# Performance work log

Hardware: AMD Instinct MI355X
Metric: run time of the kernel (lower is better)

The kernel has to match this reference:

```python
import jax, jax.numpy as jnp
import numpy as np

B, S, D, H = 4, 2048, 1024, 16
DK = D // H

def setup_inputs() -> dict:
    key = jax.random.key(0)
    ks = jax.random.split(key, 12)
    s = 1.0 / np.sqrt(D)
    return {
        "query": jax.random.normal(ks[0], (B, S, D), jnp.float32),
        "key": jax.random.normal(ks[1], (B, S, D), jnp.float32),
        "value": jax.random.normal(ks[2], (B, S, D), jnp.float32),
        "mask": jax.random.randint(ks[3], (B, S, S), 0, 2, jnp.int32),
        "Wq": jax.random.normal(ks[4], (D, D), jnp.float32) * s,
        "bq": jnp.zeros((D,), jnp.float32),
        "Wk": jax.random.normal(ks[5], (D, D), jnp.float32) * s,
        "bk": jnp.zeros((D,), jnp.float32),
        "Wv": jax.random.normal(ks[6], (D, D), jnp.float32) * s,
        "bv": jnp.zeros((D,), jnp.float32),
        "Wo": jax.random.normal(ks[7], (D, D), jnp.float32) * s,
        "bo": jnp.zeros((D,), jnp.float32),
    }

def _split_heads(x):
    b, s, _ = x.shape
    return x.reshape(b, s, H, DK).transpose(0, 2, 1, 3)  # [b,h,s,dk]

def reference(query, key, value, mask, Wq, bq, Wk, bk, Wv, bv, Wo, bo):
    # torch nn.Linear: y = x @ W.T + b
    Q = _split_heads(query @ Wq.T + bq)
    K = _split_heads(key @ Wk.T + bk)
    V = _split_heads(value @ Wv.T + bv)
    scores = jnp.einsum('bhqd,bhkd->bhqk', Q, K) / np.sqrt(DK)
    scores = jnp.where(mask[:, None, :, :] == 0, jnp.float32(-1e9), scores)
    probs = jax.nn.softmax(scores, axis=-1)
    attn = jnp.einsum('bhqk,bhkd->bhqd', probs, V)
    out = attn.transpose(0, 2, 1, 3).reshape(query.shape[0], -1, H * DK)
    return out @ Wo.T + bo
```

## Files before the change

kernel.cpp:

```cpp
#include <hip/hip_runtime.h>

typedef __attribute__((ext_vector_type(8))) short short8;
typedef __attribute__((ext_vector_type(8))) unsigned short ushort8_t;
typedef __attribute__((ext_vector_type(4))) float floatx4;
typedef __attribute__((ext_vector_type(2))) _Float16 half2_t;
typedef __attribute__((ext_vector_type(4))) _Float16 half4;
typedef __attribute__((ext_vector_type(8))) _Float16 half8;

#define B_ 4
#define S_ 2048
#define D_ 1024
#define H_ 16
#define DK_ 64
#define BS_ (B_ * S_)

union V8u { half8 v8; half4 v4[2]; };
union H16 { _Float16 h; unsigned short u; };

typedef const __attribute__((address_space(1))) void* gvp;
typedef __attribute__((address_space(3))) void* lvp;

static __device__ __forceinline__ unsigned short f2bf(float f) {
  union { float f; unsigned int u; } x; x.f = f;
  unsigned int r = x.u + 0x7fffu + ((x.u >> 16) & 1u);
  return (unsigned short)(r >> 16);
}

static __device__ __forceinline__ half2_t pk_f16(float a, float b) {
  return __builtin_bit_cast(half2_t, __builtin_amdgcn_cvt_pkrtz(a, b));
}

__global__ void cast3_kernel(const float* __restrict__ a, const float* __restrict__ b,
                             const float* __restrict__ c,
                             unsigned short* __restrict__ oa, unsigned short* __restrict__ ob,
                             unsigned short* __restrict__ oc, int n4) {
  int i = blockIdx.x * blockDim.x + threadIdx.x;
  int w = blockIdx.y;
  const float* src = (w == 0) ? a : (w == 1) ? b : c;
  unsigned short* dst = (w == 0) ? oa : (w == 1) ? ob : oc;
  if (i < n4) {
    float4 v = ((const float4*)src)[i];
    ushort4 o;
    o.x = f2bf(v.x); o.y = f2bf(v.y); o.z = f2bf(v.z); o.w = f2bf(v.w);
    ((ushort4*)dst)[i] = o;
  }
}

__global__ void cast4_kernel(const float* __restrict__ a, const float* __restrict__ b,
                             const float* __restrict__ c, const float* __restrict__ d,
                             unsigned short* __restrict__ oa, unsigned short* __restrict__ ob,
                             unsigned short* __restrict__ oc, unsigned short* __restrict__ od, int n4) {
  int i = blockIdx.x * blockDim.x + threadIdx.x;
  int w = blockIdx.y;
  const float* src = (w == 0) ? a : (w == 1) ? b : (w == 2) ? c : d;
  unsigned short* dst = (w == 0) ? oa : (w == 1) ? ob : (w == 2) ? oc : od;
  if (i < n4) {
    float4 v = ((const float4*)src)[i];
    ushort4 o;
    o.x = f2bf(v.x); o.y = f2bf(v.y); o.z = f2bf(v.z); o.w = f2bf(v.w);
    ((ushort4*)dst)[i] = o;
  }
}

__global__ void pack_mask(const int* __restrict__ mask, unsigned long long* __restrict__ bits) {
  int i = blockIdx.x * blockDim.x + threadIdx.x;
  unsigned long long m = __ballot(mask[i] != 0);
  if ((threadIdx.x & 63) == 0) bits[i >> 6] = m;
}

__global__ void transpose_v(const unsigned short* __restrict__ Vh, unsigned short* __restrict__ Vt) {
  __shared__ unsigned short T[64][72];
  int bh = blockIdx.y;
  int s0 = blockIdx.x * 64;
  int tid = threadIdx.x;
  int r = tid >> 3, c = (tid & 7) * 8;
  const unsigned short* src = Vh + ((size_t)bh * S_ + s0) * DK_;
#pragma unroll
  for (int p = 0; p < 2; ++p)
    *(uint4*)(&T[r + p * 32][c]) = *(const uint4*)(src + (size_t)(r + p * 32) * DK_ + c);
  __syncthreads();
  unsigned short* dst = Vt + (size_t)bh * DK_ * S_;
#pragma unroll
  for (int p = 0; p < 2; ++p) {
    int d = r + p * 32;
    ushort8_t o;
#pragma unroll
    for (int i = 0; i < 8; ++i) {
      int pos = c + i;
      int th = pos >> 5, rem = pos & 31;
      int q4 = rem >> 3, rem2 = rem & 7;
      int t = th * 2 + (rem2 >> 2), j = rem2 & 3;
      int k = t * 16 + q4 * 4 + j;
      o[i] = T[k][d];
    }
    *(ushort8_t*)(dst + (size_t)d * S_ + s0 + c) = o;
  }
}

__device__ __forceinline__ void gemm_core(
    const unsigned short* __restrict__ X, const unsigned short* __restrict__ W,
    const float* __restrict__ bias, void* __restrict__ Y,
    float scale, int mode, int bm, int bn,
    unsigned short* As, unsigned short* Bs)
{
  constexpr int K = D_, N = D_;
  int tid = threadIdx.x;
  int wave = tid >> 6, lane = tid & 63, quad = lane >> 4, li = lane & 15;
  int wm = wave >> 1, wn = wave & 1;
  int srow = lane >> 3;
  int scol = ((lane & 7) ^ srow) * 8;
  const unsigned short* gA = X + (size_t)(bm * 128 + wave * 32 + srow) * K + scol;
  const unsigned short* gB = W + (size_t)(bn * 128 + wave * 32 + srow) * K + scol;

  auto stage = [&](int buf, int k0) {
#pragma unroll
    for (int j = 0; j < 4; ++j) {
      __builtin_amdgcn_global_load_lds((gvp)(gA + (size_t)(j * 8) * K + k0),
          (lvp)(As + buf * 8192 + wave * 2048 + j * 512), 16, 0, 0);
      __builtin_amdgcn_global_load_lds((gvp)(gB + (size_t)(j * 8) * K + k0),
          (lvp)(Bs + buf * 8192 + wave * 2048 + j * 512), 16, 0, 0);
    }
  };

  floatx4 acc[4][4] = {};
  stage(0, 0);
  constexpr int NK = K / 64;
  for (int i = 0; i < NK; ++i) {
    int buf = i & 1;
    __syncthreads();
    if (i + 1 < NK) stage(buf ^ 1, (i + 1) * 64);
    short8 af[2][4], bf[2][4];
#pragma unroll
    for (int s2 = 0; s2 < 2; ++s2)
#pragma unroll
      for (int t = 0; t < 4; ++t) {
        int slot = ((s2 * 4 + quad) ^ (li & 7)) * 8;
        af[s2][t] = *(const short8*)(&As[buf * 8192 + (wm * 64 + t * 16 + li) * 64 + slot]);
        bf[s2][t] = *(const short8*)(&Bs[buf * 8192 + (wn * 64 + t * 16 + li) * 64 + slot]);
      }
#pragma unroll
    for (int s2 = 0; s2 < 2; ++s2)
#pragma unroll
      for (int mt = 0; mt < 4; ++mt)
#pragma unroll
        for (int nt = 0; nt < 4; ++nt)
          acc[mt][nt] = __builtin_amdgcn_mfma_f32_16x16x32_bf16(af[s2][mt], bf[s2][nt], acc[mt][nt], 0, 0, 0);
  }

#pragma unroll
  for (int nt = 0; nt < 4; ++nt) {
    int n = bn * 128 + wn * 64 + nt * 16 + li;
    float bv = bias[n];
#pragma unroll
    for (int mt = 0; mt < 4; ++mt) {
#pragma unroll
      for (int r = 0; r < 4; ++r) {
        int m = bm * 128 + wm * 64 + mt * 16 + quad * 4 + r;
        float v = (acc[mt][nt][r] + bv) * scale;
        if (mode == 1) {
          ((float*)Y)[(size_t)m * N + n] = v;
        } else {
          int b = m >> 11, s = m & 2047, h = n >> 6, dk = n & 63;
          size_t idx = (((size_t)(b * H_ + h)) * S_ + s) * DK_ + dk;
          if (mode == 0) {
            ((unsigned short*)Y)[idx] = f2bf(v);
          } else {
            H16 hv; hv.h = (_Float16)v;
            ((unsigned short*)Y)[idx] = hv.u;
          }
        }
      }
    }
  }
}

__global__ __launch_bounds__(256) void gemm_qkv(
    const unsigned short* __restrict__ Xq, const unsigned short* __restrict__ Xk,
    const unsigned short* __restrict__ Xv,
    const unsigned short* __restrict__ Wq, const unsigned short* __restrict__ Wk,
    const unsigned short* __restrict__ Wv,
    const float* __restrict__ bq, const float* __restrict__ bk, const float* __restrict__ bv,
    unsigned short* __restrict__ Qh, unsigned short* __restrict__ Kh,
    unsigned short* __restrict__ Vh, float sc)
{
  __shared__ __align__(16) unsigned short As[2 * 8192];
  __shared__ __align__(16) unsigned short Bs[2 * 8192];
  int z = blockIdx.z;
  const unsigned short* X = (z == 0) ? Xq : (z == 1) ? Xk : Xv;
  const unsigned short* W = (z == 0) ? Wq : (z == 1) ? Wk : Wv;
  const float* bias = (z == 0) ? bq : (z == 1) ? bk : bv;
  void* Y = (z == 0) ? (void*)Qh : (z == 1) ? (void*)Kh : (void*)Vh;
  float scale = (z == 0) ? sc : 1.0f;
  int mode = (z == 2) ? 2 : 0;
  gemm_core(X, W, bias, Y, scale, mode, blockIdx.y, blockIdx.x, As, Bs);
}

__global__ __launch_bounds__(256) void gemm_out(
    const unsigned short* __restrict__ X, const unsigned short* __restrict__ W,
    const float* __restrict__ bias, float* __restrict__ Y)
{
  __shared__ __align__(16) unsigned short As[2 * 8192];
  __shared__ __align__(16) unsigned short Bs[2 * 8192];
  gemm_core(X, W, bias, Y, 1.0f, 1, blockIdx.y, blockIdx.x, As, Bs);
}

__global__ __launch_bounds__(256) void attn_kernel(
    const unsigned short* __restrict__ Qh,
    const unsigned short* __restrict__ Kh,
    const _Float16* __restrict__ Vt,
    const unsigned long long* __restrict__ mbits,
    unsigned short* __restrict__ attnb)
{
  __shared__ __align__(16) unsigned short Ks[2 * 4096];
  __shared__ __align__(16) unsigned short Vs[2 * 4096];

  int tid = threadIdx.x;
  int wave = tid >> 6, lane = tid & 63, quad = lane >> 4, li = lane & 15;

  int blk = blockIdx.x;
  int xcd = blk & 7, slot7 = blk >> 3;
  int bh = xcd * 8 + (slot7 >> 4);
  int qb = slot7 & 15;
  int b = bh >> 4, h = bh & 15;
  int qbase = qb * 128 + wave * 32;
  const size_t hq = (size_t)bh * S_ * DK_;

  short8 aQ[2][2];
#pragma unroll
  for (int qs = 0; qs < 2; ++qs)
#pragma unroll
    for (int s2 = 0; s2 < 2; ++s2)
      aQ[qs][s2] = *(const short8*)(Qh + hq + (size_t)(qbase + qs * 16 + li) * DK_ + s2 * 32 + quad * 8);

  floatx4 o[2][4] = {};
  float l[2] = {0.f, 0.f};

  const unsigned long long* mrow = mbits + ((size_t)b * S_ + qbase + li) * (S_ / 64);

  int srow = lane >> 3;
  int scol = ((lane & 7) ^ srow) * 8;
  const unsigned short* gK = Kh + hq + (size_t)(wave * 16 + srow) * DK_ + scol;
  const _Float16* gV = Vt + ((size_t)bh * 64 + wave * 16 + srow) * S_ + scol;

  auto stage = [&](int buf, int k0) {
#pragma unroll
    for (int j = 0; j < 2; ++j) {
      __builtin_amdgcn_global_load_lds((gvp)(gK + (size_t)(k0 + j * 8) * DK_),
          (lvp)(Ks + buf * 4096 + wave * 1024 + j * 512), 16, 0, 0);
      __builtin_amdgcn_global_load_lds((gvp)(gV + (size_t)(j * 8) * S_ + k0),
          (lvp)(Vs + buf * 4096 + wave * 1024 + j * 512), 16, 0, 0);
    }
  };

  stage(0, 0);
  unsigned long long mw0c = mrow[0];
  unsigned long long mw1c = mrow[16 * (S_ / 64)];

  constexpr int NK = S_ / 64;
  for (int i = 0; i < NK; ++i) {
    int buf = i & 1;
    __syncthreads();
    if (i + 1 < NK) stage(buf ^ 1, (i + 1) * 64);
    unsigned long long mw0n = 0, mw1n = 0;
    if (i + 1 < NK) { mw0n = mrow[i + 1]; mw1n = mrow[16 * (S_ / 64) + i + 1]; }

    short8 bK[4][2];
#pragma unroll
    for (int t = 0; t < 4; ++t)
#pragma unroll
      for (int s2 = 0; s2 < 2; ++s2)
        bK[t][s2] = *(const short8*)(&Ks[buf * 4096 + (t * 16 + li) * 64 + (((s2 * 4 + quad) ^ (li & 7)) * 8)]);

    V8u vv[4][2];
#pragma unroll
    for (int dt = 0; dt < 4; ++dt)
#pragma unroll
      for (int tp = 0; tp < 2; ++tp)
        vv[dt][tp].v8 = *(const half8*)((const _Float16*)&Vs[buf * 4096 + (dt * 16 + li) * 64 + (((tp * 4 + quad) ^ (li & 7)) * 8)]);

    floatx4 sc[4][2] = {};
#pragma unroll
    for (int s2 = 0; s2 < 2; ++s2)
#pragma unroll
      for (int t = 0; t < 4; ++t)
#pragma unroll
        for (int qs = 0; qs < 2; ++qs)
          sc[t][qs] = __builtin_amdgcn_mfma_f32_16x16x32_bf16(bK[t][s2], aQ[qs][s2], sc[t][qs], 0, 0, 0);

    unsigned long long sh0 = mw0c >> (quad * 4);
    unsigned long long sh1 = mw1c >> (quad * 4);

    half4 aP[4][2];
#pragma unroll
    for (int t = 0; t < 4; ++t)
#pragma unroll
      for (int qs = 0; qs < 2; ++qs) {
        unsigned nb = (unsigned)(((qs ? sh1 : sh0) >> (t * 16)) & 15u);
        float p0 = (nb & 1u)        ? exp2f(sc[t][qs][0]) : 0.f;
        float p1 = ((nb >> 1) & 1u) ? exp2f(sc[t][qs][1]) : 0.f;
        float p2 = ((nb >> 2) & 1u) ? exp2f(sc[t][qs][2]) : 0.f;
        float p3 = ((nb >> 3) & 1u) ? exp2f(sc[t][qs][3]) : 0.f;
        l[qs] += (p0 + p1) + (p2 + p3);
        half2_t plo = pk_f16(p0, p1);
        half2_t phi = pk_f16(p2, p3);
        aP[t][qs] = __builtin_shufflevector(plo, phi, 0, 1, 2, 3);
      }

#pragma unroll
    for (int t = 0; t < 4; ++t)
#pragma unroll
      for (int qs = 0; qs < 2; ++qs)
#pragma unroll
        for (int dt = 0; dt < 4; ++dt)
          o[qs][dt] = __builtin_amdgcn_mfma_f32_16x16x16f16(aP[t][qs], vv[dt][t >> 1].v4[t & 1], o[qs][dt], 0, 0, 0);

    mw0c = mw0n; mw1c = mw1n;
  }

  float inv[2];
#pragma unroll
  for (int qs = 0; qs < 2; ++qs) {
    float lf = l[qs];
    lf += __shfl_xor(lf, 16, 64);
    lf += __shfl_xor(lf, 32, 64);
    inv[qs] = 1.0f / lf;
  }
#pragma unroll
  for (int qs = 0; qs < 2; ++qs)
#pragma unroll
    for (int r = 0; r < 4; ++r) {
      float ir = __shfl(inv[qs], quad * 4 + r, 64);
      size_t row = (size_t)b * S_ + qbase + qs * 16 + quad * 4 + r;
#pragma unroll
      for (int dt = 0; dt < 4; ++dt)
        attnb[row * D_ + h * DK_ + dt * 16 + li] = f2bf(o[qs][dt][r] * ir);
    }
}

extern "C" void kernel_launch(void* const* d_in, const int* in_sizes, int n_in,
                              void* d_out, int out_size, void* d_ws, size_t ws_size,
                              hipStream_t stream) {
  const float* query = (const float*)d_in[0];
  const float* key   = (const float*)d_in[1];
  const float* value = (const float*)d_in[2];
  const int*   mask  = (const int*)d_in[3];
  const float* Wq = (const float*)d_in[4];
  const float* bq = (const float*)d_in[5];
  const float* Wk = (const float*)d_in[6];
  const float* bk = (const float*)d_in[7];
  const float* Wv = (const float*)d_in[8];
  const float* bv = (const float*)d_in[9];
  const float* Wo = (const float*)d_in[10];
  const float* bo = (const float*)d_in[11];
  float* out = (float*)d_out;

  char* ws = (char*)d_ws;
  size_t off = 0;
  auto alloc = [&](size_t bytes) -> void* {
    void* p = ws + off;
    off += (bytes + 255) & ~(size_t)255;
    return p;
  };
  unsigned short* Xq    = (unsigned short*)alloc((size_t)BS_ * D_ * 2);
  unsigned short* Xk    = (unsigned short*)alloc((size_t)BS_ * D_ * 2);
  unsigned short* Xv    = (unsigned short*)alloc((size_t)BS_ * D_ * 2);
  unsigned short* Wqb   = (unsigned short*)alloc((size_t)D_ * D_ * 2);
  unsigned short* Wkb   = (unsigned short*)alloc((size_t)D_ * D_ * 2);
  unsigned short* Wvb   = (unsigned short*)alloc((size_t)D_ * D_ * 2);
  unsigned short* Wob   = (unsigned short*)alloc((size_t)D_ * D_ * 2);
  unsigned short* Qh    = (unsigned short*)alloc((size_t)BS_ * D_ * 2);
  unsigned short* Kh    = (unsigned short*)alloc((size_t)BS_ * D_ * 2);
  unsigned short* Vh    = (unsigned short*)alloc((size_t)BS_ * D_ * 2);
  unsigned short* Vt    = (unsigned short*)alloc((size_t)BS_ * D_ * 2);
  unsigned short* attnb = (unsigned short*)alloc((size_t)BS_ * D_ * 2);
  unsigned long long* mbits = (unsigned long long*)alloc((size_t)B_ * S_ * (S_ / 64) * 8);

  const float SC = 0.18033688011112042f;

  pack_mask<<<(B_ * S_ * S_) / 256, 256, 0, stream>>>(mask, mbits);

  int wn4 = D_ * D_ / 4;
  cast4_kernel<<<dim3(wn4 / 256, 4), 256, 0, stream>>>(Wq, Wk, Wv, Wo, Wqb, Wkb, Wvb, Wob, wn4);

  int xn4 = BS_ * D_ / 4;
  cast3_kernel<<<dim3(xn4 / 256, 3), 256, 0, stream>>>(query, key, value, Xq, Xk, Xv, xn4);

  gemm_qkv<<<dim3(D_ / 128, BS_ / 128, 3), 256, 0, stream>>>(
      Xq, Xk, Xv, Wqb, Wkb, Wvb, bq, bk, bv, Qh, Kh, Vh, SC);

  transpose_v<<<dim3(S_ / 64, B_ * H_), 256, 0, stream>>>(Vh, Vt);

  attn_kernel<<<dim3(8 * 8 * 16), 256, 0, stream>>>(Qh, Kh, (const _Float16*)Vt, mbits, attnb);

  gemm_out<<<dim3(D_ / 128, BS_ / 128), 256, 0, stream>>>(attnb, Wob, bo, out);
}
```

Baseline: 504.9 us.

## Mask probabilities via LDS bitmask LUT and compute row sums with MFMA

Replaces the per-element conditional exp2 with an unconditional exp2, then applies the mask by ANDing the packed fp16 pairs with a 16-entry LDS lookup table keyed on the 4-bit mask nibble. The softmax denominator now comes from an extra MFMA of P against a ones vector instead of scalar adds followed by cross-lane shuffles. The change also raises wave priority around the MFMA sections and unrolls the key loop by two. Together these cut VALU and branch work in the softmax section, at the cost of one LDS read per nibble and about 11% more MFMA issues per tile.

```diff
diff --git a/kernel.cpp b/kernel.cpp
--- a/kernel.cpp
+++ b/kernel.cpp
@@ -6,6 +6,7 @@
 typedef __attribute__((ext_vector_type(2))) _Float16 half2_t;
 typedef __attribute__((ext_vector_type(4))) _Float16 half4;
 typedef __attribute__((ext_vector_type(8))) _Float16 half8;
+typedef __attribute__((ext_vector_type(2))) unsigned int uint2v;
 
 #define B_ 4
 #define S_ 2048
@@ -213,9 +214,18 @@
 {
   __shared__ __align__(16) unsigned short Ks[2 * 4096];
   __shared__ __align__(16) unsigned short Vs[2 * 4096];
+  __shared__ __align__(8) uint2v mlut[16];
 
   int tid = threadIdx.x;
   int wave = tid >> 6, lane = tid & 63, quad = lane >> 4, li = lane & 15;
+
+  if (tid < 16) {
+    unsigned nb = (unsigned)tid;
+    uint2v m;
+    m.x = (nb & 1u ? 0x0000FFFFu : 0u) | (nb & 2u ? 0xFFFF0000u : 0u);
+    m.y = (nb & 4u ? 0x0000FFFFu : 0u) | (nb & 8u ? 0xFFFF0000u : 0u);
+    mlut[tid] = m;
+  }
 
   int blk = blockIdx.x;
   int xcd = blk & 7, slot7 = blk >> 3;
@@ -233,7 +243,8 @@
       aQ[qs][s2] = *(const short8*)(Qh + hq + (size_t)(qbase + qs * 16 + li) * DK_ + s2 * 32 + quad * 8);
 
   floatx4 o[2][4] = {};
-  float l[2] = {0.f, 0.f};
+  floatx4 lacc[2] = {};
+  const half4 ones4 = {(_Float16)1.f, (_Float16)1.f, (_Float16)1.f, (_Float16)1.f};
 
   const unsigned long long* mrow = mbits + ((size_t)b * S_ + qbase + li) * (S_ / 64);
 
@@ -257,6 +268,7 @@
   unsigned long long mw1c = mrow[16 * (S_ / 64)];
 
   constexpr int NK = S_ / 64;
+#pragma unroll 2
   for (int i = 0; i < NK; ++i) {
     int buf = i & 1;
     __syncthreads();
@@ -279,6 +291,7 @@
         vv[dt][tp].v8 = *(const half8*)((const _Float16*)&Vs[buf * 4096 + (dt * 16 + li) * 64 + (((tp * 4 + quad) ^ (li & 7)) * 8)]);
 
     floatx4 sc[4][2] = {};
+    __builtin_amdgcn_s_setprio(1);
 #pragma unroll
     for (int s2 = 0; s2 < 2; ++s2)
 #pragma unroll
@@ -286,6 +299,7 @@
 #pragma unroll
         for (int qs = 0; qs < 2; ++qs)
           sc[t][qs] = __builtin_amdgcn_mfma_f32_16x16x32_bf16(bK[t][s2], aQ[qs][s2], sc[t][qs], 0, 0, 0);
+    __builtin_amdgcn_s_setprio(0);
 
     unsigned long long sh0 = mw0c >> (quad * 4);
     unsigned long long sh1 = mw1c >> (quad * 4);
@@ -296,40 +310,37 @@
 #pragma unroll
       for (int qs = 0; qs < 2; ++qs) {
         unsigned nb = (unsigned)(((qs ? sh1 : sh0) >> (t * 16)) & 15u);
-        float p0 = (nb & 1u)        ? exp2f(sc[t][qs][0]) : 0.f;
-        float p1 = ((nb >> 1) & 1u) ? exp2f(sc[t][qs][1]) : 0.f;
-        float p2 = ((nb >> 2) & 1u) ? exp2f(sc[t][qs][2]) : 0.f;
-        float p3 = ((nb >> 3) & 1u) ? exp2f(sc[t][qs][3]) : 0.f;
-        l[qs] += (p0 + p1) + (p2 + p3);
-        half2_t plo = pk_f16(p0, p1);
-        half2_t phi = pk_f16(p2, p3);
-        aP[t][qs] = __builtin_shufflevector(plo, phi, 0, 1, 2, 3);
+        uint2v mm = mlut[nb];
+        float p0 = exp2f(sc[t][qs][0]);
+        float p1 = exp2f(sc[t][qs][1]);
+        float p2 = exp2f(sc[t][qs][2]);
+        float p3 = exp2f(sc[t][qs][3]);
+        unsigned lo = __builtin_bit_cast(unsigned, pk_f16(p0, p1)) & mm.x;
+        unsigned hi = __builtin_bit_cast(unsigned, pk_f16(p2, p3)) & mm.y;
+        uint2v pp; pp.x = lo; pp.y = hi;
+        aP[t][qs] = __builtin_bit_cast(half4, pp);
       }
 
+    __builtin_amdgcn_s_setprio(1);
 #pragma unroll
     for (int t = 0; t < 4; ++t)
 #pragma unroll
-      for (int qs = 0; qs < 2; ++qs)
+      for (int qs = 0; qs < 2; ++qs) {
+        lacc[qs] = __builtin_amdgcn_mfma_f32_16x16x16f16(aP[t][qs], ones4, lacc[qs], 0, 0, 0);
 #pragma unroll
         for (int dt = 0; dt < 4; ++dt)
           o[qs][dt] = __builtin_amdgcn_mfma_f32_16x16x16f16(aP[t][qs], vv[dt][t >> 1].v4[t & 1], o[qs][dt], 0, 0, 0);
+      }
+    __builtin_amdgcn_s_setprio(0);
 
     mw0c = mw0n; mw1c = mw1n;
   }
 
-  float inv[2];
-#pragma unroll
-  for (int qs = 0; qs < 2; ++qs) {
-    float lf = l[qs];
-    lf += __shfl_xor(lf, 16, 64);
-    lf += __shfl_xor(lf, 32, 64);
-    inv[qs] = 1.0f / lf;
-  }
 #pragma unroll
   for (int qs = 0; qs < 2; ++qs)
 #pragma unroll
     for (int r = 0; r < 4; ++r) {
-      float ir = __shfl(inv[qs], quad * 4 + r, 64);
+      float ir = 1.0f / lacc[qs][r];
       size_t row = (size_t)b * S_ + qbase + qs * 16 + quad * 4 + r;
 #pragma unroll
       for (int dt = 0; dt < 4; ++dt)
```

Measured after the change: 479.7 us. 1.05x faster.
